# Kernel tuning notes

Hardware: AMD Instinct MI355X
Metric: run time of the kernel (lower is better)

The kernel has to match this reference:

```python
import jax, jax.numpy as jnp
import numpy as np

N, B, H, IN_DIM, OUT_DIM = 1024, 16, 64, 2, 12
BACK, STEP = 2.0, 1.0
HIST = int(BACK / STEP)          # history steps = 2
FUR = int(OUT_DIM / STEP)        # future integration steps = 12
THRES = 1e-3                     # edge threshold (thres in __init__)
NBINS = HIST + 1                 # quantized delay bins: 0..HIST steps
N_KNOTS = 11                     # spline intervals (12 knots)


def setup_inputs() -> dict:
    key = jax.random.key(0)
    ks = iter(jax.random.split(key, 32))
    f32 = jnp.float32

    def rn(shape, scale):
        return (scale * jax.random.normal(next(ks), shape, dtype=f32))

    inp = {
        "A": jax.random.uniform(next(ks), (N, N), dtype=f32),
        "all_delay": jax.random.uniform(next(ks), (N, N), dtype=f32) * BACK,
        "coeff_a": rn((B, N, N_KNOTS, IN_DIM), 0.1),
        "coeff_b": rn((B, N, N_KNOTS, IN_DIM), 0.1),
        "coeff_c": rn((B, N, N_KNOTS, IN_DIM), 0.1),
        "coeff_d": rn((B, N, N_KNOTS, IN_DIM), 0.1),
        "node_emb": rn((N, H), 0.1),
        "i2h_W1": rn((IN_DIM, H), 1.0 / np.sqrt(IN_DIM)),
        "i2h_b1": jnp.zeros((H,), f32),
        "i2h_W2": rn((H, H * HIST), 1.0 / np.sqrt(H)),
        "i2h_b2": jnp.zeros((H * HIST,), f32),
        "dde_Wm": rn((H, H), 1.0 / np.sqrt(H)),
        "dde_Ws": rn((H, H), 1.0 / np.sqrt(H)),
        "dde_Wx": rn((IN_DIM, H), 1.0 / np.sqrt(IN_DIM)),
        "dde_b": jnp.zeros((H,), f32),
        "reg_W1": rn((H, H // 2), 1.0 / np.sqrt(H)),
        "reg_b1": jnp.zeros((H // 2,), f32),
        "reg_W2": rn((H // 2, 1), 1.0 / np.sqrt(H // 2)),
        "reg_b2": jnp.zeros((1,), f32),
        "pred_W1": rn((H, H // 2), 1.0 / np.sqrt(H)),
        "pred_b1": jnp.zeros((H // 2,), f32),
        "pred_W2": rn((H // 2, OUT_DIM), 1.0 / np.sqrt(H // 2)),
        "pred_b2": jnp.zeros((OUT_DIM,), f32),
    }
    return inp


def _spline(coeffs, t):
    """Natural cubic spline: value and derivative at scalar time t.
    knots at times BACK + arange(12); coeffs [B,N,11,IN]."""
    a, b, c, d = coeffs
    idx = jnp.clip(jnp.floor(t - BACK).astype(jnp.int32), 0, a.shape[2] - 1)
    frac = t - BACK - idx.astype(a.dtype)
    A_ = jnp.take(a, idx, axis=2)
    B_ = jnp.take(b, idx, axis=2)
    C_ = jnp.take(c, idx, axis=2)
    D_ = jnp.take(d, idx, axis=2)
    val = A_ + frac * (B_ + frac * (C_ + frac * D_))
    der = B_ + frac * (2.0 * C_ + 3.0 * frac * D_)
    return val, der  # each [B,N,IN]


def _forward(A, all_delay, coeff_a, coeff_b, coeff_c, coeff_d, node_emb,
             i2h_W1, i2h_b1, i2h_W2, i2h_b2,
             dde_Wm, dde_Ws, dde_Wx, dde_b,
             reg_W1, reg_b1, reg_W2, reg_b2,
             pred_W1, pred_b1, pred_W2, pred_b2):
    coeffs = (coeff_a, coeff_b, coeff_c, coeff_d)
    # --- dynamic graph build (dense, thresholded) ---
    sem = jax.nn.softmax(jax.nn.relu(node_emb @ node_emb.T), axis=1)     # semantic_A
    Ah = A + jnp.eye(N, dtype=A.dtype)                                   # normalized adj
    dinv = jax.lax.rsqrt(Ah.sum(axis=1))
    spatial = dinv[:, None] * Ah * dinv[None, :]
    Ac = sem + spatial
    W = jnp.where(Ac > THRES, Ac, 0.0)                                   # edge weights
    dsteps = jnp.round(jnp.clip(all_delay, 0.0, BACK) / STEP).astype(jnp.int32)
    Wbins = jnp.stack([jnp.where(dsteps == d, W, 0.0) for d in range(NBINS)])  # [NBINS,N,N]

    # --- history hidden states from initial spline value ---
    x0, _ = _spline(coeffs, jnp.asarray(BACK, A.dtype))                  # [B,N,IN]
    hid = jax.nn.relu(x0 @ i2h_W1 + i2h_b1) @ i2h_W2 + i2h_b2            # [B,N,H*HIST]
    hist = hid.reshape(B, N, HIST, H).transpose(1, 2, 0, 3)              # [N,HIST,B,H]
    S = jnp.concatenate([hist, jnp.zeros((N, FUR, B, H), hist.dtype)], axis=1)
    h0 = hist[:, HIST - 1]                                               # y0 [N,B,H]

    def step(carry, k):
        S, h = carry
        idx = HIST - 1 + k  # current time index in S
        agg = jnp.zeros_like(h)
        for d in range(NBINS):  # delayed message passing per delay bin
            sd = jax.lax.dynamic_slice_in_dim(S, jnp.maximum(idx - d, 0), 1, axis=1)[:, 0]
            agg = agg + jnp.einsum('ji,jbh->ibh', Wbins[d], sd)
        t = BACK + STEP * k.astype(h.dtype)
        _, dx = _spline(coeffs, t)                                       # control derivative
        dx = dx.transpose(1, 0, 2)                                       # [N,B,IN]
        pre = agg @ dde_Wm + h @ dde_Ws + dx @ dde_Wx + dde_b
        h_new = h + STEP * (jnp.tanh(pre) - h)                           # Euler step of DDE
        S = jax.lax.dynamic_update_slice_in_dim(S, h_new[:, None], idx + 1, axis=1)
        return (S, h_new), h_new

    (_, _), y_hidden = jax.lax.scan(step, (S, h0), jnp.arange(FUR))      # [FUR,N,B,H]

    reg = (jax.nn.relu(y_hidden @ reg_W1 + reg_b1) @ reg_W2 + reg_b2)[..., 0]  # [FUR,N,B]
    ts = BACK + jnp.arange(OUT_DIM, dtype=A.dtype)
    tgt = jax.vmap(lambda t: _spline(coeffs, t)[0][:, :, 0].T)(ts)       # [OUT,N,B]
    diff = reg - tgt
    ad = jnp.abs(diff)
    reg_loss = jnp.where(ad < 1.0, 0.5 * diff * diff, ad - 0.5).mean()

    y_pred = (jax.nn.relu(y_hidden[-1] @ pred_W1 + pred_b1) @ pred_W2 + pred_b2)
    y_pred = y_pred.transpose(1, 0, 2)                                   # [B,N,OUT]
    return y_pred, reg_loss


def reference(A, all_delay, coeff_a, coeff_b, coeff_c, coeff_d, node_emb,
              i2h_W1, i2h_b1, i2h_W2, i2h_b2,
              dde_Wm, dde_Ws, dde_Wx, dde_b,
              reg_W1, reg_b1, reg_W2, reg_b2,
              pred_W1, pred_b1, pred_W2, pred_b2):
    return _forward(A, all_delay, coeff_a, coeff_b, coeff_c, coeff_d, node_emb,
                    i2h_W1, i2h_b1, i2h_W2, i2h_b2,
                    dde_Wm, dde_Ws, dde_Wx, dde_b,
                    reg_W1, reg_b1, reg_W2, reg_b2,
                    pred_W1, pred_b1, pred_W2, pred_b2)
```

## Files before the change

kernel.cpp:

```cpp
#include <hip/hip_runtime.h>
#include <cstddef>
#include <cstdint>

#define NN 1024
#define BB 16
#define NKNOTS 11

typedef __attribute__((ext_vector_type(8))) short short8_v;
typedef __attribute__((ext_vector_type(4))) float f32x4;
typedef __attribute__((ext_vector_type(8))) unsigned short ushort8_v;
typedef __attribute__((ext_vector_type(4))) unsigned short ushort4_v;
typedef __attribute__((ext_vector_type(4))) unsigned int uint4_v;

#define WTHI_OFF  ((size_t)0)
#define STHI_OFF  ((size_t)6 << 20)
#define STLO_OFF  ((size_t)14 << 20)
#define WGT_OFF   ((size_t)22 << 20)
#define SYNC_OFF  (((size_t)22 << 20) + 16384)
#define LOSS_OFF  (SYNC_OFF + 2048)
#define Z_OFF     (LOSS_OFF + 256)
#define DINV_OFF  (Z_OFF + 4096)

#define AGGS   0
#define AGGH   17408
#define AGGL   25600
#define HH_    33792
#define HL_    41984
#define HT32   50176
#define REDS   66560
#define PL1    68608
#define WGT_L  98304

__device__ __forceinline__ unsigned short f2bf(float x) {
  unsigned int u = __float_as_uint(x);
  return (unsigned short)((u + 0x7FFFu + ((u >> 16) & 1u)) >> 16);
}
__device__ __forceinline__ float bf2f(unsigned short h) {
  return __uint_as_float(((unsigned int)h) << 16);
}
__device__ __forceinline__ void gload16(const void* g, void* l) {
  __builtin_amdgcn_global_load_lds(
      (const __attribute__((address_space(1))) unsigned int*)g,
      (__attribute__((address_space(3))) unsigned int*)l, 16, 0, 0);
}

__global__ __launch_bounds__(256) void rowstats_kernel(
    const float* __restrict__ emb, const float* __restrict__ A,
    float* __restrict__ Z, float* __restrict__ dinv)
{
  const int j = blockIdx.x;
  const int tid = threadIdx.x;
  __shared__ float ej[64];
  __shared__ float r1[256], r2[256];
  if (tid < 64) ej[tid] = emb[j * 64 + tid];
  __syncthreads();
  float zs = 0.f, as = 0.f;
  for (int i = tid; i < NN; i += 256) {
    const float4* er = (const float4*)(emb + (size_t)i * 64);
    float dot = 0.f;
#pragma unroll
    for (int q = 0; q < 16; ++q) {
      float4 e = er[q];
      dot += e.x * ej[q * 4 + 0] + e.y * ej[q * 4 + 1] +
             e.z * ej[q * 4 + 2] + e.w * ej[q * 4 + 3];
    }
    zs += expf(fmaxf(dot, 0.f));
    as += A[(size_t)j * NN + i];
  }
  r1[tid] = zs; r2[tid] = as;
  __syncthreads();
  for (int s = 128; s > 0; s >>= 1) {
    if (tid < s) { r1[tid] += r1[tid + s]; r2[tid] += r2[tid + s]; }
    __syncthreads();
  }
  if (tid == 0) {
    Z[j] = r1[0];
    dinv[j] = rsqrtf(r2[0] + 1.0f);
  }
}

__global__ __launch_bounds__(256) void build_wt_kernel(
    const float* __restrict__ emb, const float* __restrict__ A,
    const float* __restrict__ delay, const float* __restrict__ Z,
    const float* __restrict__ dinv, unsigned short* __restrict__ WThi)
{
  __shared__ float eI[64][65];
  __shared__ float eJ[64][65];
  __shared__ float wS[64][65];
  __shared__ unsigned char dS[64][64];
  __shared__ float diS[64];

  const int tid = threadIdx.x;
  const int it = blockIdx.x >> 4, jt = blockIdx.x & 15;
  const int i0 = it * 64, j0 = jt * 64;

  for (int q = tid; q < 4096; q += 256) {
    int r = q >> 6, c = q & 63;
    eI[r][c] = emb[(size_t)(i0 + r) * 64 + c];
    eJ[r][c] = emb[(size_t)(j0 + r) * 64 + c];
  }
  if (tid < 64) diS[tid] = dinv[i0 + tid];
  __syncthreads();

  const int jj = tid >> 2, iig = (tid & 3) * 16;
  float dotv[16];
#pragma unroll
  for (int m = 0; m < 16; ++m) dotv[m] = 0.f;
#pragma unroll 4
  for (int h4 = 0; h4 < 16; ++h4) {
    float4 a = *(const float4*)&eJ[jj][h4 * 4];
#pragma unroll
    for (int m = 0; m < 16; ++m) {
      float4 bb = *(const float4*)&eI[iig + m][h4 * 4];
      dotv[m] += a.x * bb.x + a.y * bb.y + a.z * bb.z + a.w * bb.w;
    }
  }
  const float Zj = Z[j0 + jj], dj = dinv[j0 + jj];
  const float* Ap = A + (size_t)(j0 + jj) * NN + i0 + iig;
  const float* Dp = delay + (size_t)(j0 + jj) * NN + i0 + iig;
#pragma unroll
  for (int m = 0; m < 16; ++m) {
    float aji = Ap[m] + ((i0 + iig + m) == (j0 + jj) ? 1.f : 0.f);
    float ac = expf(fmaxf(dotv[m], 0.f)) / Zj + dj * diS[iig + m] * aji;
    float w = (ac > 0.001f) ? ac : 0.f;
    float dl = fminf(fmaxf(Dp[m], 0.f), 2.f);
    wS[jj][iig + m] = w;
    dS[jj][iig + m] = (unsigned char)(int)rintf(dl);
  }
  __syncthreads();

  const int iw = tid >> 2, jg = (tid & 3) * 16;
#pragma unroll
  for (int d0 = 0; d0 < 3; ++d0) {
    ushort8_v P0, P1;
#pragma unroll
    for (int m = 0; m < 8; ++m) {
      int j1 = jg + m, j2 = jg + 8 + m;
      P0[m] = f2bf((dS[j1][iw] == d0) ? wS[j1][iw] : 0.f);
      P1[m] = f2bf((dS[j2][iw] == d0) ? wS[j2][iw] : 0.f);
    }
    size_t off = ((size_t)d0 << 20) + (size_t)(i0 + iw) * NN + j0 + jg;
    *(ushort8_v*)(WThi + off) = P0;
    *(ushort8_v*)(WThi + off + 8) = P1;
  }
}

__global__ __launch_bounds__(256) void init_s_kernel(
    const float* __restrict__ ca, const float* __restrict__ W1,
    const float* __restrict__ b1, const float* __restrict__ W2,
    const float* __restrict__ b2,
    unsigned short* __restrict__ SThi, unsigned short* __restrict__ STlo,
    const float* __restrict__ Wm, const float* __restrict__ Wsm,
    unsigned short* __restrict__ wgt)
{
  const int bid = blockIdx.x;
  const int tid = threadIdx.x;
  if (bid >= 256) {
    int e = (bid - 256) * 256 + tid;
    int n = e >> 7, kk = e & 127;
    float v = (kk < 64) ? Wm[kk * 64 + n] : Wsm[(kk - 64) * 64 + n];
    wgt[n * 128 + (((kk >> 3) ^ (n & 15)) << 3) + (kk & 7)] = f2bf(v);
    return;
  }
  __shared__ float l1S[64][65];
  __shared__ float W2S[64][128];
  __shared__ float hidS[64][129];

  const int nt = bid >> 4, b = bid & 15;
  const int n0 = nt * 64;

  for (int q = tid; q < 2048; q += 256)
    ((float4*)&W2S[0][0])[q] = ((const float4*)W2)[q];

  {
    const int n = tid >> 2, hb = (tid & 3) * 16;
    float2 x = *(const float2*)(ca + ((size_t)(b * NN + n0 + n) * NKNOTS) * 2);
#pragma unroll
    for (int m = 0; m < 16; ++m) {
      int h = hb + m;
      l1S[n][h] = fmaxf(x.x * W1[h] + x.y * W1[64 + h] + b1[h], 0.f);
    }
  }
  __syncthreads();
  {
    const int nn = tid & 63, o0 = (tid >> 6) * 32;
    float hid[32];
#pragma unroll
    for (int o = 0; o < 32; ++o) hid[o] = b2[o0 + o];
    for (int h = 0; h < 64; ++h) {
      float lv = l1S[nn][h];
#pragma unroll
      for (int o = 0; o < 32; ++o) hid[o] = fmaf(lv, W2S[h][o0 + o], hid[o]);
    }
#pragma unroll
    for (int o = 0; o < 32; ++o) hidS[nn][o0 + o] = hid[o];
  }
  __syncthreads();
  {
    const int r = tid >> 1, hf = tid & 1;
    const int t = r >> 6, hh = r & 63;
    size_t off = ((size_t)t << 20) + (size_t)(b * 64 + hh) * NN + n0 + hf * 32;
    ushort8_v H[4], L[4];
#pragma unroll
    for (int q = 0; q < 4; ++q)
#pragma unroll
      for (int m = 0; m < 8; ++m) {
        float v = hidS[hf * 32 + q * 8 + m][r];
        unsigned short hv = f2bf(v);
        H[q][m] = hv; L[q][m] = f2bf(v - bf2f(hv));
      }
#pragma unroll
    for (int q = 0; q < 4; ++q) {
      *(ushort8_v*)(SThi + off + q * 8) = H[q];
      *(ushort8_v*)(STlo + off + q * 8) = L[q];
    }
  }
}

__global__ __launch_bounds__(512, 2) void scan_kernel(
    const unsigned short* __restrict__ WThi,
    unsigned short* __restrict__ SThi, unsigned short* __restrict__ STlo,
    const unsigned short* __restrict__ wgt, unsigned int* __restrict__ syncc,
    const float* __restrict__ Wx, const float* __restrict__ db,
    const float* __restrict__ cb, const float* __restrict__ cc,
    const float* __restrict__ cd, const float* __restrict__ ca,
    const float* __restrict__ rW1, const float* __restrict__ rb1,
    const float* __restrict__ rW2, const float* __restrict__ rb2,
    const float* __restrict__ pW1, const float* __restrict__ pb1,
    const float* __restrict__ pW2, const float* __restrict__ pb2,
    float* __restrict__ out, float* __restrict__ loss)
{
  __shared__ __align__(16) char smem[114688];
  __shared__ float sWx[128];
  __shared__ float sdb[64];

  const int tid  = threadIdx.x;
  const int lane = tid & 63;
  const int w    = tid >> 6;
  const int bid  = blockIdx.x;
  const int i_t = bid >> 4;
  const int b   = bid & 15;
  const int i0 = i_t * 64, c0 = b * 64;

  const int wr = (w >> 1) & 1, wc = w & 1, kh = w >> 2;
  const int g = lane >> 4, l15 = lane & 15, sw = l15 & 7;

  if (tid < 128) sWx[tid] = Wx[tid];
  else if (tid < 192) sdb[tid - 128] = db[tid - 128];

  gload16(wgt + (size_t)tid * 8,        smem + WGT_L + tid * 16);
  gload16(wgt + 4096 + (size_t)tid * 8, smem + WGT_L + 8192 + tid * 16);

  const int s_r = tid >> 4;
  const int s_s = tid & 15;
  const int s_c = (s_s & 8) | ((s_s & 7) ^ (s_r & 7));
  const int rA0 = (wr * 32 + l15) * 256;
  const int rB0 = 16384 + (wc * 32 + l15) * 256;

  float (*aggS)[68] = (float (*)[68])(smem + AGGS);

  for (int k = 0; k < 12; ++k) {
    f32x4 acc[2][2];
#pragma unroll
    for (int fr = 0; fr < 2; ++fr)
#pragma unroll
      for (int fc = 0; fc < 2; ++fc)
        acc[fr][fc] = (f32x4){0.f, 0.f, 0.f, 0.f};

    auto stage = [&](int t) {
      const int d = t >> 3, t8 = t & 7;
      int td = k + 1 - d; if (td < 0) td = 0;
      const unsigned short* Ab = WThi + ((size_t)d << 20) +
                                 (size_t)(i0 + s_r) * NN + t8 * 128;
      const unsigned short* Bb = SThi + ((size_t)(td & 3) << 20) +
                                 (size_t)(c0 + s_r) * NN + t8 * 128;
      char* dst = smem + (t % 3) * 32768;
      gload16(Ab + s_c * 8,                  dst + tid * 16);
      gload16(Ab + (size_t)32 * NN + s_c * 8, dst + 8192 + tid * 16);
      gload16(Bb + s_c * 8,                  dst + 16384 + tid * 16);
      gload16(Bb + (size_t)32 * NN + s_c * 8, dst + 24576 + tid * 16);
    };

    stage(0); stage(1);
    asm volatile("s_waitcnt vmcnt(4)" ::: "memory");
    __builtin_amdgcn_s_barrier();

    for (int t = 0; t < 24; ++t) {
      if (t < 22) stage(t + 2);
      const char* bp = smem + (t % 3) * 32768;
#pragma unroll
      for (int ks = 0; ks < 2; ++ks) {
        const int s16 = ((kh << 3) | ((ks * 4 + g) ^ sw)) << 4;
        short8_v a0 = *(const short8_v*)(bp + rA0 + s16);
        short8_v a1 = *(const short8_v*)(bp + rA0 + 4096 + s16);
        short8_v b0 = *(const short8_v*)(bp + rB0 + s16);
        short8_v b1 = *(const short8_v*)(bp + rB0 + 4096 + s16);
        acc[0][0] = __builtin_amdgcn_mfma_f32_16x16x32_bf16(a0, b0, acc[0][0], 0, 0, 0);
        acc[0][1] = __builtin_amdgcn_mfma_f32_16x16x32_bf16(a0, b1, acc[0][1], 0, 0, 0);
        acc[1][0] = __builtin_amdgcn_mfma_f32_16x16x32_bf16(a1, b0, acc[1][0], 0, 0, 0);
        acc[1][1] = __builtin_amdgcn_mfma_f32_16x16x32_bf16(a1, b1, acc[1][1], 0, 0, 0);
      }
      __builtin_amdgcn_sched_barrier(0);
      if (t < 22) {
        asm volatile("s_waitcnt vmcnt(4)" ::: "memory");
        __builtin_amdgcn_s_barrier();
      } else if (t == 22) {
        asm volatile("s_waitcnt vmcnt(0)" ::: "memory");
        __builtin_amdgcn_s_barrier();
      }
    }

    if (kh == 0) {
#pragma unroll
      for (int fr = 0; fr < 2; ++fr)
#pragma unroll
        for (int fc = 0; fc < 2; ++fc)
#pragma unroll
          for (int rr = 0; rr < 4; ++rr)
            aggS[wr * 32 + fr * 16 + g * 4 + rr][wc * 32 + fc * 16 + l15] = acc[fr][fc][rr];
    }
    __syncthreads();
    if (kh == 1) {
#pragma unroll
      for (int fr = 0; fr < 2; ++fr)
#pragma unroll
        for (int fc = 0; fc < 2; ++fc)
#pragma unroll
          for (int rr = 0; rr < 4; ++rr)
            aggS[wr * 32 + fr * 16 + g * 4 + rr][wc * 32 + fc * 16 + l15] += acc[fr][fc][rr];
    }
    __syncthreads();

    {
      const int row = tid >> 3, c8 = tid & 7;
      const float* src = &aggS[row][c8 * 8];
      ushort8_v H, L;
#pragma unroll
      for (int q = 0; q < 8; ++q) {
        float f = src[q];
        unsigned short hv = f2bf(f);
        H[q] = hv; L[q] = f2bf(f - bf2f(hv));
      }
      const int pos = (c8 ^ (row & 7)) << 4;
      *(ushort8_v*)(smem + AGGH + row * 128 + pos) = H;
      *(ushort8_v*)(smem + AGGL + row * 128 + pos) = L;
    }
    {
      const int cl = tid >> 3, ich = (tid & 7) * 8;
      size_t off = ((size_t)((k + 1) & 3) << 20) + (size_t)(c0 + cl) * NN + (i0 + ich);
      ushort8_v h8 = *(const ushort8_v*)(SThi + off);
      ushort8_v l8 = *(const ushort8_v*)(STlo + off);
#pragma unroll
      for (int q = 0; q < 8; ++q) {
        int i = ich + q;
        int byo = i * 128 + ((((cl >> 3) ^ (i & 7))) << 4) + (cl & 7) * 2;
        *(unsigned short*)(smem + HH_ + byo) = h8[q];
        *(unsigned short*)(smem + HL_ + byo) = l8[q];
      }
    }
    __syncthreads();

    const int mr = w & 3, nc = w >> 2;
    f32x4 pacc[2];
    pacc[0] = (f32x4){0.f, 0.f, 0.f, 0.f};
    pacc[1] = (f32x4){0.f, 0.f, 0.f, 0.f};
#pragma unroll
    for (int ks = 0; ks < 4; ++ks) {
      const int base = (ks < 2) ? AGGH : HH_;
      const int ks2 = ks & 1;
      const int cxa = ((ks2 * 4 + g) ^ (l15 & 7)) << 4;
      const char* ra = smem + base + (mr * 16 + l15) * 128 + cxa;
      short8_v aH = *(const short8_v*)ra;
      short8_v aL = *(const short8_v*)(ra + 8192);
#pragma unroll
      for (int fc = 0; fc < 2; ++fc) {
        const int n = (nc * 2 + fc) * 16 + l15;
        const int cxb = ((ks * 4 + g) ^ l15) << 4;
        short8_v bv = *(const short8_v*)(smem + WGT_L + n * 256 + cxb);
        pacc[fc] = __builtin_amdgcn_mfma_f32_16x16x32_bf16(aH, bv, pacc[fc], 0, 0, 0);
        pacc[fc] = __builtin_amdgcn_mfma_f32_16x16x32_bf16(aL, bv, pacc[fc], 0, 0, 0);
      }
    }
    __syncthreads();

    const int ksp = (k < 11) ? k : 10;
    float hn[2][4];
#pragma unroll
    for (int rr = 0; rr < 4; ++rr) {
      int iG = i0 + mr * 16 + g * 4 + rr;
      size_t cbase = ((size_t)(b * NN + iG) * NKNOTS + ksp) * 2;
      float dx0 = cb[cbase + 0], dx1 = cb[cbase + 1];
      if (k == 11) {
        dx0 += 2.f * cc[cbase + 0] + 3.f * cd[cbase + 0];
        dx1 += 2.f * cc[cbase + 1] + 3.f * cd[cbase + 1];
      }
#pragma unroll
      for (int fc = 0; fc < 2; ++fc) {
        int hcol = (nc * 2 + fc) * 16 + l15;
        float pre = pacc[fc][rr] + dx0 * sWx[hcol] + dx1 * sWx[64 + hcol] + sdb[hcol];
        hn[fc][rr] = tanhf(pre);
      }
    }
#pragma unroll
    for (int fc = 0; fc < 2; ++fc) {
      int hcol = (nc * 2 + fc) * 16 + l15;
      int iG0 = i0 + mr * 16 + g * 4;
      size_t off2 = ((size_t)((k + 2) & 3) << 20) + (size_t)(c0 + hcol) * NN + iG0;
      ushort4_v H4, L4;
      uint4_v pk;
#pragma unroll
      for (int rr = 0; rr < 4; ++rr) {
        unsigned short hv = f2bf(hn[fc][rr]);
        unsigned short lv = f2bf(hn[fc][rr] - bf2f(hv));
        H4[rr] = hv; L4[rr] = lv;
        pk[rr] = ((unsigned int)hv << 16) | lv;
      }
      *(ushort4_v*)(SThi + off2) = H4;
      *(ushort4_v*)(STlo + off2) = L4;
      const int ci = mr * 4 + g;
      *(uint4_v*)(smem + HT32 + hcol * 256 + ((ci ^ (hcol & 15)) << 4)) = pk;
    }
    asm volatile("s_waitcnt vmcnt(0)" ::: "memory");
    __syncthreads();
    if (tid == 0) atomicAdd(&syncc[b * 32 + k], 1u);

    {
      const int ii = tid & 63, mg4 = (tid >> 6) * 4;
      float s0 = rb1[mg4], s1 = rb1[mg4 + 1], s2 = rb1[mg4 + 2], s3 = rb1[mg4 + 3];
#pragma unroll 8
      for (int h = 0; h < 64; ++h) {
        unsigned int v = *(const unsigned int*)(smem + HT32 + h * 256 +
                           ((((ii >> 2) ^ (h & 15))) << 4) + (ii & 3) * 4);
        float f = bf2f((unsigned short)(v >> 16)) + bf2f((unsigned short)(v & 0xffff));
        float4 wv = *(const float4*)(rW1 + h * 32 + mg4);
        s0 = fmaf(f, wv.x, s0); s1 = fmaf(f, wv.y, s1);
        s2 = fmaf(f, wv.z, s2); s3 = fmaf(f, wv.w, s3);
      }
      float4 r2v = *(const float4*)(rW2 + mg4);
      float rp = fmaxf(s0, 0.f) * r2v.x + fmaxf(s1, 0.f) * r2v.y +
                 fmaxf(s2, 0.f) * r2v.z + fmaxf(s3, 0.f) * r2v.w;
      float* redS = (float*)(smem + REDS);
      redS[(tid >> 6) * 64 + ii] = rp;
      __syncthreads();
      if (tid < 64) {
        float rv = rb2[0];
#pragma unroll
        for (int m = 0; m < 8; ++m) rv += redS[m * 64 + tid];
        int iG = i0 + tid;
        size_t tb = ((size_t)(b * NN + iG) * NKNOTS + ksp) * 2;
        float tgt = ca[tb];
        if (k == 11) tgt += cb[tb] + cc[tb] + cd[tb];
        float dv = rv - tgt;
        float ad = fabsf(dv);
        float hub = (ad < 1.f) ? 0.5f * dv * dv : (ad - 0.5f);
        hub += __shfl_down(hub, 32);
        hub += __shfl_down(hub, 16);
        hub += __shfl_down(hub, 8);
        hub += __shfl_down(hub, 4);
        hub += __shfl_down(hub, 2);
        hub += __shfl_down(hub, 1);
        if (tid == 0) atomicAdd(loss, hub);
      }
    }

    if (k == 11) {
      __syncthreads();
      const int ii = tid & 63, mg4 = (tid >> 6) * 4;
      float s0 = pb1[mg4], s1 = pb1[mg4 + 1], s2 = pb1[mg4 + 2], s3 = pb1[mg4 + 3];
#pragma unroll 8
      for (int h = 0; h < 64; ++h) {
        unsigned int v = *(const unsigned int*)(smem + HT32 + h * 256 +
                           ((((ii >> 2) ^ (h & 15))) << 4) + (ii & 3) * 4);
        float f = bf2f((unsigned short)(v >> 16)) + bf2f((unsigned short)(v & 0xffff));
        float4 wv = *(const float4*)(pW1 + h * 32 + mg4);
        s0 = fmaf(f, wv.x, s0); s1 = fmaf(f, wv.y, s1);
        s2 = fmaf(f, wv.z, s2); s3 = fmaf(f, wv.w, s3);
      }
      float* pl1 = (float*)(smem + PL1);
      pl1[ii * 32 + mg4 + 0] = fmaxf(s0, 0.f);
      pl1[ii * 32 + mg4 + 1] = fmaxf(s1, 0.f);
      pl1[ii * 32 + mg4 + 2] = fmaxf(s2, 0.f);
      pl1[ii * 32 + mg4 + 3] = fmaxf(s3, 0.f);
      __syncthreads();
#pragma unroll
      for (int rep = 0; rep < 2; ++rep) {
        int idxp = tid + rep * 512;
        if (idxp < 768) {
          int i_ = idxp / 12, o = idxp % 12;
          float s = pb2[o];
#pragma unroll
          for (int m = 0; m < 32; ++m) s = fmaf(pl1[i_ * 32 + m], pW2[m * 12 + o], s);
          out[((size_t)b * NN + (i0 + i_)) * 12 + o] = s;
        }
      }
    }

    __syncthreads();
    if (tid == 0) {
      unsigned int* ctr = &syncc[b * 32 + k];
      while (atomicAdd(ctr, 0u) < 16u) __builtin_amdgcn_s_sleep(1);
      asm volatile("buffer_inv sc0" ::: "memory");
    }
    __syncthreads();
  }
}

__global__ void finalize_kernel(const float* __restrict__ loss, float* __restrict__ out)
{
  out[196608] = loss[0] * (1.0f / 196608.0f);
}

extern "C" void kernel_launch(void* const* d_in, const int* in_sizes, int n_in,
                              void* d_out, int out_size, void* d_ws, size_t ws_size,
                              hipStream_t stream)
{
  const float* A     = (const float*)d_in[0];
  const float* delay = (const float*)d_in[1];
  const float* ca    = (const float*)d_in[2];
  const float* cb    = (const float*)d_in[3];
  const float* cc    = (const float*)d_in[4];
  const float* cd    = (const float*)d_in[5];
  const float* emb   = (const float*)d_in[6];
  const float* iW1   = (const float*)d_in[7];
  const float* ib1   = (const float*)d_in[8];
  const float* iW2   = (const float*)d_in[9];
  const float* ib2   = (const float*)d_in[10];
  const float* Wm    = (const float*)d_in[11];
  const float* Wsm   = (const float*)d_in[12];
  const float* Wx    = (const float*)d_in[13];
  const float* db    = (const float*)d_in[14];
  const float* rW1   = (const float*)d_in[15];
  const float* rb1   = (const float*)d_in[16];
  const float* rW2   = (const float*)d_in[17];
  const float* rb2   = (const float*)d_in[18];
  const float* pW1   = (const float*)d_in[19];
  const float* pb1   = (const float*)d_in[20];
  const float* pW2   = (const float*)d_in[21];
  const float* pb2   = (const float*)d_in[22];

  char* wsb = (char*)d_ws;
  float* out = (float*)d_out;
  unsigned short* WThi = (unsigned short*)(wsb + WTHI_OFF);
  unsigned short* SThi = (unsigned short*)(wsb + STHI_OFF);
  unsigned short* STlo = (unsigned short*)(wsb + STLO_OFF);
  unsigned short* wgt  = (unsigned short*)(wsb + WGT_OFF);
  unsigned int* syncc  = (unsigned int*)(wsb + SYNC_OFF);
  float* loss          = (float*)(wsb + LOSS_OFF);
  float* Z             = (float*)(wsb + Z_OFF);
  float* dinv          = (float*)(wsb + DINV_OFF);

  hipMemsetAsync(syncc, 0, 2048 + 64, stream);
  rowstats_kernel<<<NN, 256, 0, stream>>>(emb, A, Z, dinv);
  build_wt_kernel<<<256, 256, 0, stream>>>(emb, A, delay, Z, dinv, WThi);
  init_s_kernel<<<288, 256, 0, stream>>>(ca, iW1, ib1, iW2, ib2,
                                         SThi, STlo, Wm, Wsm, wgt);
  scan_kernel<<<256, 512, 0, stream>>>(
      WThi, SThi, STlo, wgt, syncc, Wx, db, cb, cc, cd, ca,
      rW1, rb1, rW2, rb2, pW1, pb1, pW2, pb2, out, loss);
  finalize_kernel<<<1, 1, 0, stream>>>(loss, out);
}
```

Baseline: 415.1 us.

## Replace three delay-split weight matrices with one weight matrix plus bitmasks

Before, build_wt wrote three dense bf16 weight matrices, one per delay bin, and the scan streamed all three every step. Now it writes one bf16 weight matrix plus a packed 3-bit-per-entry delay mask. The scan kernel rebuilds each per-delay A operand in registers by ANDing with LUT-expanded masks before the MFMAs. This cuts A-operand global traffic about threefold. In exchange it adds LDS LUT lookups and ALU masking in the inner loop, uses slightly more LDS, and restructures the k-loop to 16 stages of 64 columns.

```diff
diff --git a/kernel.cpp b/kernel.cpp
--- a/kernel.cpp
+++ b/kernel.cpp
@@ -11,8 +11,10 @@
 typedef __attribute__((ext_vector_type(8))) unsigned short ushort8_v;
 typedef __attribute__((ext_vector_type(4))) unsigned short ushort4_v;
 typedef __attribute__((ext_vector_type(4))) unsigned int uint4_v;
-
-#define WTHI_OFF  ((size_t)0)
+typedef __attribute__((ext_vector_type(2))) unsigned int uint2_v;
+
+#define WPK_OFF   ((size_t)0)
+#define M3_OFF    ((size_t)2 << 20)
 #define STHI_OFF  ((size_t)6 << 20)
 #define STLO_OFF  ((size_t)14 << 20)
 #define WGT_OFF   ((size_t)22 << 20)
@@ -29,7 +31,8 @@
 #define HT32   50176
 #define REDS   66560
 #define PL1    68608
-#define WGT_L  98304
+#define WGT_L  104448
+#define LUT_OFF 120832
 
 __device__ __forceinline__ unsigned short f2bf(float x) {
   unsigned int u = __float_as_uint(x);
@@ -42,6 +45,11 @@
   __builtin_amdgcn_global_load_lds(
       (const __attribute__((address_space(1))) unsigned int*)g,
       (__attribute__((address_space(3))) unsigned int*)l, 16, 0, 0);
+}
+__device__ __forceinline__ void gload4(const void* g, void* l) {
+  __builtin_amdgcn_global_load_lds(
+      (const __attribute__((address_space(1))) unsigned int*)g,
+      (__attribute__((address_space(3))) unsigned int*)l, 4, 0, 0);
 }
 
 __global__ __launch_bounds__(256) void rowstats_kernel(
@@ -82,7 +90,8 @@
 __global__ __launch_bounds__(256) void build_wt_kernel(
     const float* __restrict__ emb, const float* __restrict__ A,
     const float* __restrict__ delay, const float* __restrict__ Z,
-    const float* __restrict__ dinv, unsigned short* __restrict__ WThi)
+    const float* __restrict__ dinv,
+    unsigned short* __restrict__ Wpk, unsigned int* __restrict__ M3g)
 {
   __shared__ float eI[64][65];
   __shared__ float eJ[64][65];
@@ -130,19 +139,29 @@
   __syncthreads();
 
   const int iw = tid >> 2, jg = (tid & 3) * 16;
-#pragma unroll
-  for (int d0 = 0; d0 < 3; ++d0) {
-    ushort8_v P0, P1;
-#pragma unroll
-    for (int m = 0; m < 8; ++m) {
-      int j1 = jg + m, j2 = jg + 8 + m;
-      P0[m] = f2bf((dS[j1][iw] == d0) ? wS[j1][iw] : 0.f);
-      P1[m] = f2bf((dS[j2][iw] == d0) ? wS[j2][iw] : 0.f);
-    }
-    size_t off = ((size_t)d0 << 20) + (size_t)(i0 + iw) * NN + j0 + jg;
-    *(ushort8_v*)(WThi + off) = P0;
-    *(ushort8_v*)(WThi + off + 8) = P1;
-  }
+  ushort8_v P0, P1;
+#pragma unroll
+  for (int m = 0; m < 8; ++m) {
+    P0[m] = f2bf(wS[jg + m][iw]);
+    P1[m] = f2bf(wS[jg + 8 + m][iw]);
+  }
+  size_t woff = (size_t)(i0 + iw) * NN + j0 + jg;
+  *(ushort8_v*)(Wpk + woff) = P0;
+  *(ushort8_v*)(Wpk + woff + 8) = P1;
+  uint2_v mw;
+#pragma unroll
+  for (int o = 0; o < 2; ++o) {
+    unsigned int m0 = 0, m1 = 0, m2 = 0;
+#pragma unroll
+    for (int e = 0; e < 8; ++e) {
+      int dv = dS[jg + o * 8 + e][iw];
+      m0 |= (dv == 0) << e;
+      m1 |= (dv == 1) << e;
+      m2 |= (dv == 2) << e;
+    }
+    mw[o] = m0 | (m1 << 8) | (m2 << 16);
+  }
+  *(uint2_v*)(M3g + (size_t)(i0 + iw) * 128 + (j0 + jg) / 8) = mw;
 }
 
 __global__ __launch_bounds__(256) void init_s_kernel(
@@ -218,7 +237,7 @@
 }
 
 __global__ __launch_bounds__(512, 2) void scan_kernel(
-    const unsigned short* __restrict__ WThi,
+    const unsigned short* __restrict__ Wpk, const unsigned int* __restrict__ M3g,
     unsigned short* __restrict__ SThi, unsigned short* __restrict__ STlo,
     const unsigned short* __restrict__ wgt, unsigned int* __restrict__ syncc,
     const float* __restrict__ Wx, const float* __restrict__ db,
@@ -230,7 +249,7 @@
     const float* __restrict__ pW2, const float* __restrict__ pb2,
     float* __restrict__ out, float* __restrict__ loss)
 {
-  __shared__ __align__(16) char smem[114688];
+  __shared__ __align__(16) char smem[120960];
   __shared__ float sWx[128];
   __shared__ float sdb[64];
 
@@ -243,19 +262,30 @@
   const int i0 = i_t * 64, c0 = b * 64;
 
   const int wr = (w >> 1) & 1, wc = w & 1, kh = w >> 2;
-  const int g = lane >> 4, l15 = lane & 15, sw = l15 & 7;
+  const int g = lane >> 4, l15 = lane & 15;
 
   if (tid < 128) sWx[tid] = Wx[tid];
   else if (tid < 192) sdb[tid - 128] = db[tid - 128];
 
+  if (tid < 32) {
+    int n = tid >> 1, half = tid & 1;
+    unsigned int dw = half == 0
+      ? (((n & 1) ? 0xFFFFu : 0u) | ((n & 2) ? 0xFFFF0000u : 0u))
+      : (((n & 4) ? 0xFFFFu : 0u) | ((n & 8) ? 0xFFFF0000u : 0u));
+    *(unsigned int*)(smem + LUT_OFF + n * 8 + half * 4) = dw;
+  }
+
   gload16(wgt + (size_t)tid * 8,        smem + WGT_L + tid * 16);
   gload16(wgt + 4096 + (size_t)tid * 8, smem + WGT_L + 8192 + tid * 16);
-
-  const int s_r = tid >> 4;
-  const int s_s = tid & 15;
-  const int s_c = (s_s & 8) | ((s_s & 7) ^ (s_r & 7));
-  const int rA0 = (wr * 32 + l15) * 256;
-  const int rB0 = 16384 + (wc * 32 + l15) * 256;
+  __syncthreads();
+
+  const int s_row = tid >> 3;
+  const int s_ch  = tid & 7;
+  const int s_cx  = (s_ch ^ (s_row & 7)) * 8;
+  const int koff  = kh * 4 + g;
+  const int s16   = (koff ^ (l15 & 7)) << 4;
+  const int rowA0 = wr * 32 + l15;
+  const int rB0   = 10240 + (wc * 32 + l15) * 128 + s16;
 
   float (*aggS)[68] = (float (*)[68])(smem + AGGS);
 
@@ -268,47 +298,61 @@
         acc[fr][fc] = (f32x4){0.f, 0.f, 0.f, 0.f};
 
     auto stage = [&](int t) {
-      const int d = t >> 3, t8 = t & 7;
-      int td = k + 1 - d; if (td < 0) td = 0;
-      const unsigned short* Ab = WThi + ((size_t)d << 20) +
-                                 (size_t)(i0 + s_r) * NN + t8 * 128;
-      const unsigned short* Bb = SThi + ((size_t)(td & 3) << 20) +
-                                 (size_t)(c0 + s_r) * NN + t8 * 128;
-      char* dst = smem + (t % 3) * 32768;
-      gload16(Ab + s_c * 8,                  dst + tid * 16);
-      gload16(Ab + (size_t)32 * NN + s_c * 8, dst + 8192 + tid * 16);
-      gload16(Bb + s_c * 8,                  dst + 16384 + tid * 16);
-      gload16(Bb + (size_t)32 * NN + s_c * 8, dst + 24576 + tid * 16);
+      const int jc = t << 6;
+      char* dst = smem + (t % 3) * 34816;
+      gload16(Wpk + (size_t)(i0 + s_row) * NN + jc + s_cx, dst + tid * 16);
+      gload4(M3g + (size_t)(i0 + s_row) * 128 + (jc >> 3) + s_ch,
+             dst + 8192 + tid * 4);
+#pragma unroll
+      for (int d = 0; d < 3; ++d) {
+        int td = k + 1 - d; if (td < 0) td = 0;
+        gload16(SThi + ((size_t)(td & 3) << 20) +
+                    (size_t)(c0 + s_row) * NN + jc + s_cx,
+                dst + 10240 + d * 8192 + tid * 16);
+      }
     };
 
     stage(0); stage(1);
-    asm volatile("s_waitcnt vmcnt(4)" ::: "memory");
+    asm volatile("s_waitcnt vmcnt(5)" ::: "memory");
     __builtin_amdgcn_s_barrier();
 
-    for (int t = 0; t < 24; ++t) {
-      if (t < 22) stage(t + 2);
-      const char* bp = smem + (t % 3) * 32768;
-#pragma unroll
-      for (int ks = 0; ks < 2; ++ks) {
-        const int s16 = ((kh << 3) | ((ks * 4 + g) ^ sw)) << 4;
-        short8_v a0 = *(const short8_v*)(bp + rA0 + s16);
-        short8_v a1 = *(const short8_v*)(bp + rA0 + 4096 + s16);
-        short8_v b0 = *(const short8_v*)(bp + rB0 + s16);
-        short8_v b1 = *(const short8_v*)(bp + rB0 + 4096 + s16);
+    for (int t = 0; t < 16; ++t) {
+      if (t < 14) stage(t + 2);
+      const char* bp = smem + (t % 3) * 34816;
+      short8_v w0 = *(const short8_v*)(bp + rowA0 * 128 + s16);
+      short8_v w1 = *(const short8_v*)(bp + (rowA0 + 16) * 128 + s16);
+      unsigned int m0 = *(const unsigned int*)(bp + 8192 + rowA0 * 32 + koff * 4);
+      unsigned int m1 = *(const unsigned int*)(bp + 8192 + (rowA0 + 16) * 32 + koff * 4);
+#pragma unroll
+      for (int d = 0; d < 3; ++d) {
+        unsigned int mb0 = (m0 >> (8 * d)) & 0xFF;
+        unsigned int mb1 = (m1 >> (8 * d)) & 0xFF;
+        uint2_v lo0 = *(const uint2_v*)(smem + LUT_OFF + (mb0 & 15) * 8);
+        uint2_v hi0 = *(const uint2_v*)(smem + LUT_OFF + (mb0 >> 4) * 8);
+        uint2_v lo1 = *(const uint2_v*)(smem + LUT_OFF + (mb1 & 15) * 8);
+        uint2_v hi1 = *(const uint2_v*)(smem + LUT_OFF + (mb1 >> 4) * 8);
+        short8_v a0 = w0, a1 = w1;
+        unsigned int* a0p = (unsigned int*)&a0;
+        unsigned int* a1p = (unsigned int*)&a1;
+        a0p[0] &= lo0[0]; a0p[1] &= lo0[1]; a0p[2] &= hi0[0]; a0p[3] &= hi0[1];
+        a1p[0] &= lo1[0]; a1p[1] &= lo1[1]; a1p[2] &= hi1[0]; a1p[3] &= hi1[1];
+        short8_v b0 = *(const short8_v*)(bp + d * 8192 + rB0);
+        short8_v b1 = *(const short8_v*)(bp + d * 8192 + rB0 + 16 * 128);
         acc[0][0] = __builtin_amdgcn_mfma_f32_16x16x32_bf16(a0, b0, acc[0][0], 0, 0, 0);
         acc[0][1] = __builtin_amdgcn_mfma_f32_16x16x32_bf16(a0, b1, acc[0][1], 0, 0, 0);
         acc[1][0] = __builtin_amdgcn_mfma_f32_16x16x32_bf16(a1, b0, acc[1][0], 0, 0, 0);
         acc[1][1] = __builtin_amdgcn_mfma_f32_16x16x32_bf16(a1, b1, acc[1][1], 0, 0, 0);
       }
       __builtin_amdgcn_sched_barrier(0);
-      if (t < 22) {
-        asm volatile("s_waitcnt vmcnt(4)" ::: "memory");
+      if (t < 14) {
+        asm volatile("s_waitcnt vmcnt(5)" ::: "memory");
         __builtin_amdgcn_s_barrier();
-      } else if (t == 22) {
+      } else if (t == 14) {
         asm volatile("s_waitcnt vmcnt(0)" ::: "memory");
         __builtin_amdgcn_s_barrier();
       }
     }
+    __syncthreads();
 
     if (kh == 0) {
 #pragma unroll
@@ -540,7 +584,8 @@
 
   char* wsb = (char*)d_ws;
   float* out = (float*)d_out;
-  unsigned short* WThi = (unsigned short*)(wsb + WTHI_OFF);
+  unsigned short* Wpk  = (unsigned short*)(wsb + WPK_OFF);
+  unsigned int*  M3g   = (unsigned int*)(wsb + M3_OFF);
   unsigned short* SThi = (unsigned short*)(wsb + STHI_OFF);
   unsigned short* STlo = (unsigned short*)(wsb + STLO_OFF);
   unsigned short* wgt  = (unsigned short*)(wsb + WGT_OFF);
@@ -551,11 +596,11 @@
 
   hipMemsetAsync(syncc, 0, 2048 + 64, stream);
   rowstats_kernel<<<NN, 256, 0, stream>>>(emb, A, Z, dinv);
-  build_wt_kernel<<<256, 256, 0, stream>>>(emb, A, delay, Z, dinv, WThi);
+  build_wt_kernel<<<256, 256, 0, stream>>>(emb, A, delay, Z, dinv, Wpk, M3g);
   init_s_kernel<<<288, 256, 0, stream>>>(ca, iW1, ib1, iW2, ib2,
                                          SThi, STlo, Wm, Wsm, wgt);
   scan_kernel<<<256, 512, 0, stream>>>(
-      WThi, SThi, STlo, wgt, syncc, Wx, db, cb, cc, cd, ca,
+      Wpk, M3g, SThi, STlo, wgt, syncc, Wx, db, cb, cc, cd, ca,
       rW1, rb1, rW2, rb2, pW1, pb1, pW2, pb2, out, loss);
   finalize_kernel<<<1, 1, 0, stream>>>(loss, out);
 }
```

After: 391.7 us. -5.6%, faster.
